# Optimization experiments

Measured on AMD Instinct MI355X. Metric: run time of the kernel, lower is better.

Reference implementation:

```python
import jax, jax.numpy as jnp
import numpy as np

B, CIN, COUT, WDIM, RES, K = 16, 512, 512, 512, 64, 3
LRELU_SLOPE = 0.2
ACT_GAIN = np.sqrt(2.0).astype(np.float32)  # def_gain for 'lrelu'


def setup_inputs() -> dict:
    key = jax.random.key(0)
    ks = jax.random.split(key, 7)
    return {
        "x": jax.random.normal(ks[0], (B, CIN, RES, RES), dtype=jnp.float32),
        "w": jax.random.normal(ks[1], (B, WDIM), dtype=jnp.float32),
        "weight": jax.random.normal(ks[2], (COUT, CIN, K, K), dtype=jnp.float32),
        "affine_w": jax.random.normal(ks[3], (CIN, WDIM), dtype=jnp.float32),
        "affine_b": jnp.ones((CIN,), dtype=jnp.float32),  # bias_init=1
        "bias": jnp.zeros((COUT,), dtype=jnp.float32),
        "noise_const": jax.random.normal(ks[4], (RES, RES), dtype=jnp.float32),
        "noise_strength": jnp.float32(0.1),
    }


def reference(x, w, weight, affine_w, affine_b, bias, noise_const, noise_strength):
    # affine: FullyConnectedLayer with weight_gain = 1/sqrt(w_dim)
    wg = jnp.float32(1.0 / np.sqrt(WDIM))
    styles = w @ (affine_w * wg).T + affine_b  # [B, CIN]

    # fused modulated conv2d (demodulate=True, fused_modconv=True, up=down=1)
    wm = weight[None] * styles[:, None, :, None, None]  # [B, COUT, CIN, K, K]
    dcoefs = jax.lax.rsqrt(jnp.sum(wm * wm, axis=(2, 3, 4)) + 1e-8)  # [B, COUT]
    wm = wm * dcoefs[:, :, None, None, None]

    # grouped conv trick: groups = batch
    xg = x.reshape(1, B * CIN, RES, RES)
    wgk = wm.reshape(B * COUT, CIN, K, K)
    pad = K // 2
    y = jax.lax.conv_general_dilated(
        xg, wgk, window_strides=(1, 1), padding=[(pad, pad), (pad, pad)],
        dimension_numbers=("NCHW", "OIHW", "NCHW"), feature_group_count=B,
    ).reshape(B, COUT, RES, RES)

    # const noise injection
    y = y + noise_const * noise_strength

    # bias_act: bias + leaky_relu + gain (conv_clamp=None, gain=1.0)
    y = jax.nn.leaky_relu(y + bias[None, :, None, None], LRELU_SLOPE) * ACT_GAIN
    return y
```

## Files before the change

kernel.cpp:

```cpp
#include <hip/hip_runtime.h>

#define BATCH 16
#define CIN 512
#define COUT 512
#define RES 64

typedef __attribute__((ext_vector_type(8))) short bf16x8;
typedef __attribute__((ext_vector_type(4))) float f32x4;

__device__ __align__(16) unsigned short g_zero[64];

static __device__ __forceinline__ unsigned short f2bf(float f) {
    unsigned int u = __float_as_uint(f);
    u += 0x7fffu + ((u >> 16) & 1u);
    return (unsigned short)(u >> 16);
}

static __device__ __forceinline__ void gload16(const void* g, void* l) {
    __builtin_amdgcn_global_load_lds(
        (const __attribute__((address_space(1))) void*)g,
        (__attribute__((address_space(3))) void*)l, 16, 0, 0);
}

__global__ void k_prep1(const float* __restrict__ w, const float* __restrict__ aw,
                        const float* __restrict__ ab, const float* __restrict__ weight,
                        float* __restrict__ styles, unsigned short* __restrict__ wA,
                        float* __restrict__ wsq) {
    if (blockIdx.x < 2048) {
        int wid  = (blockIdx.x * blockDim.x + threadIdx.x) >> 6;
        int lane = threadIdx.x & 63;
        int b = wid >> 9, i = wid & 511;
        const float* wrow = w + b * 512;
        const float* arow = aw + (size_t)i * 512;
        float acc = 0.f;
        for (int k = lane; k < 512; k += 64) acc += wrow[k] * arow[k];
        for (int off = 32; off; off >>= 1) acc += __shfl_down(acc, off, 64);
        if (lane == 0) styles[wid] = acc * 0.04419417382415922f + ab[i];
    } else {
        int o = blockIdx.x - 2048;
        __shared__ float lw[4608];
        for (int idx = threadIdx.x; idx < 4608; idx += 256)
            lw[idx] = weight[(size_t)o * 4608 + idx];
        __syncthreads();
        int i = threadIdx.x * 2;
        float sq0 = 0.f, sq1 = 0.f;
#pragma unroll
        for (int t = 0; t < 9; ++t) {
            float v0 = lw[i * 9 + t], v1 = lw[(i + 1) * 9 + t];
            sq0 += v0 * v0; sq1 += v1 * v1;
            unsigned* dst = (unsigned*)(wA + (((size_t)t * COUT + o) << 9));
            dst[threadIdx.x] = (unsigned)f2bf(v0) | ((unsigned)f2bf(v1) << 16);
        }
        *(float2*)(wsq + ((size_t)o << 9) + i) = make_float2(sq0, sq1);
    }
}

__global__ void k_dcoefs(const float* __restrict__ wsq, const float* __restrict__ styles,
                         float* __restrict__ dcoefs) {
    int wid  = (blockIdx.x * blockDim.x + threadIdx.x) >> 6;
    int lane = threadIdx.x & 63;
    int b = wid >> 9, o = wid & 511;
    const float* srow = styles + b * 512;
    const float* qrow = wsq + ((size_t)o << 9);
    float acc = 0.f;
    for (int i = lane; i < 512; i += 64) {
        float s = srow[i];
        acc += s * s * qrow[i];
    }
    for (int off = 32; off; off >>= 1) acc += __shfl_down(acc, off, 64);
    if (lane == 0) dcoefs[wid] = rsqrtf(acc + 1e-8f);
}

__global__ void k_xpose(const float* __restrict__ x, const float* __restrict__ styles,
                        unsigned short* __restrict__ xt) {
    int bh = blockIdx.x;
    int ic = blockIdx.y;
    int b = bh >> 6, h = bh & 63;
    __shared__ float tile[32][65];
    __shared__ float st[32];
    const float* src = x + ((size_t)b * 512 + ic * 32) * 4096 + h * 64;
    if (threadIdx.x < 32) st[threadIdx.x] = styles[b * 512 + ic * 32 + threadIdx.x];
    for (int idx = threadIdx.x; idx < 512; idx += 256) {
        int c = idx >> 4, w4 = (idx & 15) * 4;
        float4 v = *(const float4*)(src + (size_t)c * 4096 + w4);
        tile[c][w4] = v.x; tile[c][w4 + 1] = v.y; tile[c][w4 + 2] = v.z; tile[c][w4 + 3] = v.w;
    }
    __syncthreads();
    int w = threadIdx.x >> 2, cg = (threadIdx.x & 3) * 8;
    bf16x8 v;
#pragma unroll
    for (int j = 0; j < 8; ++j) v[j] = (short)f2bf(tile[cg + j][w] * st[cg + j]);
    *(bf16x8*)(xt + (((size_t)bh * 64 + w) << 9) + ic * 32 + cg) = v;
}

__global__ __launch_bounds__(256, 2)
void k_conv(const unsigned short* __restrict__ wA, const unsigned short* __restrict__ xt,
            const float* __restrict__ dcoefs,
            const float* __restrict__ noise, const float* __restrict__ nstr,
            const float* __restrict__ bias, float* __restrict__ out) {
    __shared__ __align__(16) unsigned short lA[128 * 32];
    __shared__ __align__(16) unsigned short lB[128 * 32];
    const int tid = threadIdx.x;
    const int lane = tid & 63;
    const int wave = tid >> 6;

    const int lid = blockIdx.x;
    const int xcd = lid & 7, grp = lid >> 3;
    const int o_blk = grp & 3;
    const int pair = ((grp >> 2) << 3) | xcd;
    const int b = pair >> 5;
    const int o0 = o_blk * 128;
    const int p0 = (pair & 31) * 128;
    const int h0 = p0 >> 6;

    const int kqs = (lane & 3) ^ ((lane >> 3) & 3);

    const unsigned short* gA0 = wA + ((size_t)(o0 + wave * 32 + (lane >> 2))) * 512 + kqs * 8;
    const unsigned short* gA1 = gA0 + 16 * 512;
    void* ldsA0 = (void*)(lA + wave * 1024);
    void* ldsA1 = (void*)(lA + wave * 1024 + 512);
    void* ldsB0 = (void*)(lB + wave * 1024);
    void* ldsB1 = (void*)(lB + wave * 1024 + 512);

    const int fm_row = (wave >> 1) * 64 + (lane & 15);
    const int fn_row = (wave & 1) * 64 + (lane & 15);
    const int kof = (((lane >> 4) ^ ((lane >> 1) & 3)) & 3) * 8;

    f32x4 acc[4][4];
#pragma unroll
    for (int i = 0; i < 4; ++i)
#pragma unroll
        for (int j = 0; j < 4; ++j) acc[i][j] = (f32x4){0.f, 0.f, 0.f, 0.f};

    for (int t = 0; t < 9; ++t) {
        const int dy = t / 3 - 1, dx = t % 3 - 1;
        const unsigned short* gB[2];
        int adv[2];
#pragma unroll
        for (int s = 0; s < 2; ++s) {
            int pp = wave * 32 + s * 16 + (lane >> 2);
            int r = pp >> 6, w = pp & 63;
            int h = h0 + r + dy, ww = w + dx;
            bool valid = ((unsigned)h < 64u) && ((unsigned)ww < 64u);
            gB[s] = valid ? xt + (((size_t)b * 64 + h) * 64 + ww) * 512 + kqs * 8
                          : g_zero + kqs * 8;
            adv[s] = valid ? 32 : 0;
        }
        for (int i0 = 0; i0 < 16; ++i0) {
            __syncthreads();
            gload16(gA0, ldsA0);
            gload16(gA1, ldsA1);
            gload16(gB[0], ldsB0);
            gload16(gB[1], ldsB1);
            gA0 += 32; gA1 += 32; gB[0] += adv[0]; gB[1] += adv[1];
            asm volatile("s_waitcnt vmcnt(0)" ::: "memory");
            __syncthreads();

            bf16x8 af[4], bfr[4];
#pragma unroll
            for (int f = 0; f < 4; ++f)
                af[f] = *(const bf16x8*)&lA[(fm_row + f * 16) * 32 + kof];
#pragma unroll
            for (int f = 0; f < 4; ++f)
                bfr[f] = *(const bf16x8*)&lB[(fn_row + f * 16) * 32 + kof];
#pragma unroll
            for (int fm = 0; fm < 4; ++fm)
#pragma unroll
                for (int fn = 0; fn < 4; ++fn)
                    acc[fm][fn] = __builtin_amdgcn_mfma_f32_16x16x32_bf16(
                        af[fm], bfr[fn], acc[fm][fn], 0, 0, 0);
        }
        gA0 += 261632; gA1 += 261632;
    }

    const float ns = nstr[0];
    const float* dcb = dcoefs + b * 512;
#pragma unroll
    for (int fm = 0; fm < 4; ++fm) {
        int ob = o0 + (wave >> 1) * 64 + fm * 16 + (lane >> 4) * 4;
#pragma unroll
        for (int fn = 0; fn < 4; ++fn) {
            int p = p0 + (wave & 1) * 64 + fn * 16 + (lane & 15);
            float nval = noise[p] * ns;
#pragma unroll
            for (int rg = 0; rg < 4; ++rg) {
                int o = ob + rg;
                float v = acc[fm][fn][rg] * dcb[o] + nval + bias[o];
                v = (v > 0.f ? v : 0.2f * v) * 1.41421356f;
                out[((size_t)(b * COUT + o) << 12) + p] = v;
            }
        }
    }
}

__global__ void k_conv_naive(const float* __restrict__ x, const float* __restrict__ w,
                             const float* __restrict__ weight,
                             const float* __restrict__ aw, const float* __restrict__ ab,
                             const float* __restrict__ noise, const float* __restrict__ nstr,
                             const float* __restrict__ bias, float* __restrict__ out) {
    const int o = blockIdx.x, b = blockIdx.y;
    __shared__ float ss[512];
    __shared__ float red[256];
    const float* wv = w + b * 512;
    for (int i = threadIdx.x; i < 512; i += 256) {
        const float* arow = aw + (size_t)i * 512;
        float acc = 0.f;
        for (int k = 0; k < 512; ++k) acc += wv[k] * arow[k];
        ss[i] = acc * 0.04419417382415922f + ab[i];
    }
    __syncthreads();
    float part = 0.f;
    for (int i = threadIdx.x; i < 512; i += 256) {
        float s = ss[i], sq = 0.f;
#pragma unroll
        for (int k = 0; k < 9; ++k) { float v = weight[((size_t)o * 512 + i) * 9 + k]; sq += v * v; }
        part += s * s * sq;
    }
    red[threadIdx.x] = part;
    __syncthreads();
    for (int st = 128; st; st >>= 1) {
        if (threadIdx.x < st) red[threadIdx.x] += red[threadIdx.x + st];
        __syncthreads();
    }
    const float dcoef = rsqrtf(red[0] + 1e-8f);

    float acc[16];
#pragma unroll
    for (int j = 0; j < 16; ++j) acc[j] = 0.f;
    for (int i = 0; i < 512; ++i) {
        const float s = ss[i];
        float wk[9];
#pragma unroll
        for (int k = 0; k < 9; ++k) wk[k] = weight[((size_t)o * 512 + i) * 9 + k] * s;
        const float* xp = x + ((size_t)b * 512 + i) * 4096;
#pragma unroll
        for (int j = 0; j < 16; ++j) {
            const int p = (j << 8) + threadIdx.x;
            const int h = p >> 6, ww = p & 63;
            float a = acc[j];
#pragma unroll
            for (int ky = 0; ky < 3; ++ky) {
                int hh = h + ky - 1;
                if ((unsigned)hh < 64u) {
#pragma unroll
                    for (int kx = 0; kx < 3; ++kx) {
                        int wv2 = ww + kx - 1;
                        if ((unsigned)wv2 < 64u) a += wk[ky * 3 + kx] * xp[hh * 64 + wv2];
                    }
                }
            }
            acc[j] = a;
        }
    }
    const float ns = nstr[0], bs = bias[o];
#pragma unroll
    for (int j = 0; j < 16; ++j) {
        int p = (j << 8) + threadIdx.x;
        float v = acc[j] * dcoef + noise[p] * ns + bs;
        v = (v > 0.f ? v : 0.2f * v) * 1.41421356f;
        out[((size_t)(b * COUT + o) << 12) + p] = v;
    }
}

extern "C" void kernel_launch(void* const* d_in, const int* in_sizes, int n_in,
                              void* d_out, int out_size, void* d_ws, size_t ws_size,
                              hipStream_t stream) {
    const float* x   = (const float*)d_in[0];
    const float* w   = (const float*)d_in[1];
    const float* wt  = (const float*)d_in[2];
    const float* aw  = (const float*)d_in[3];
    const float* ab  = (const float*)d_in[4];
    const float* bs  = (const float*)d_in[5];
    const float* nc  = (const float*)d_in[6];
    const float* nst = (const float*)d_in[7];
    float* out = (float*)d_out;

    char* ws = (char*)d_ws;
    float* styles = (float*)ws;
    float* dcoefs = (float*)(ws + 32 * 1024);
    float* wsq    = (float*)(ws + 64 * 1024);
    unsigned short* wA = (unsigned short*)(ws + (2 << 20));
    unsigned short* xt = (unsigned short*)(ws + (2 << 20) + 4718592ull);
    const size_t need = (size_t)(2 << 20) + 4718592ull + 67108864ull;

    if (d_ws != nullptr && ws_size >= need) {
        k_prep1<<<2560, 256, 0, stream>>>(w, aw, ab, wt, styles, wA, wsq);
        k_dcoefs<<<2048, 256, 0, stream>>>(wsq, styles, dcoefs);
        k_xpose<<<dim3(1024, 16), 256, 0, stream>>>(x, styles, xt);
        k_conv<<<2048, 256, 0, stream>>>(wA, xt, dcoefs, nc, nst, bs, out);
    } else {
        k_conv_naive<<<dim3(512, 16), 256, 0, stream>>>(x, w, wt, aw, ab, nc, nst, bs, out);
    }
}
```

Measured before the change: 605.0 us.

## Rewrite conv GEMM as 256x256 tile with double-buffered LDS pipeline

The implicit-GEMM conv kernel now uses 512-thread blocks, each computing a 256x256 output tile with a K step of 64. LDS is double-buffered and the global-to-LDS loads for upcoming K tiles are interleaved with four MFMA quadrant phases, using s_setprio and explicit vmcnt waits. The aim is to hide load latency and raise arithmetic intensity per LDS byte, in place of the old single-buffered 128x128 tile that waited on every load. In exchange the kernel needs 128 KB of LDS per block, more accumulator registers, and only 512 blocks, which may reduce occupancy.

```diff
diff --git a/kernel.cpp b/kernel.cpp
--- a/kernel.cpp
+++ b/kernel.cpp
@@ -4,6 +4,7 @@
 #define CIN 512
 #define COUT 512
 #define RES 64
+#define K_TILES 72
 
 typedef __attribute__((ext_vector_type(8))) short bf16x8;
 typedef __attribute__((ext_vector_type(4))) float f32x4;
@@ -93,98 +94,184 @@
     *(bf16x8*)(xt + (((size_t)bh * 64 + w) << 9) + ic * 32 + cg) = v;
 }
 
-__global__ __launch_bounds__(256, 2)
+__global__ __launch_bounds__(512, 2)
 void k_conv(const unsigned short* __restrict__ wA, const unsigned short* __restrict__ xt,
             const float* __restrict__ dcoefs,
             const float* __restrict__ noise, const float* __restrict__ nstr,
             const float* __restrict__ bias, float* __restrict__ out) {
-    __shared__ __align__(16) unsigned short lA[128 * 32];
-    __shared__ __align__(16) unsigned short lB[128 * 32];
-    const int tid = threadIdx.x;
+    __shared__ __align__(16) unsigned short lA[2][2][8192];
+    __shared__ __align__(16) unsigned short lB[2][2][8192];
+
+    const int tid  = threadIdx.x;
     const int lane = tid & 63;
     const int wave = tid >> 6;
-
-    const int lid = blockIdx.x;
-    const int xcd = lid & 7, grp = lid >> 3;
-    const int o_blk = grp & 3;
-    const int pair = ((grp >> 2) << 3) | xcd;
-    const int b = pair >> 5;
-    const int o0 = o_blk * 128;
-    const int p0 = (pair & 31) * 128;
-    const int h0 = p0 >> 6;
-
-    const int kqs = (lane & 3) ^ ((lane >> 3) & 3);
-
-    const unsigned short* gA0 = wA + ((size_t)(o0 + wave * 32 + (lane >> 2))) * 512 + kqs * 8;
-    const unsigned short* gA1 = gA0 + 16 * 512;
-    void* ldsA0 = (void*)(lA + wave * 1024);
-    void* ldsA1 = (void*)(lA + wave * 1024 + 512);
-    void* ldsB0 = (void*)(lB + wave * 1024);
-    void* ldsB1 = (void*)(lB + wave * 1024 + 512);
-
-    const int fm_row = (wave >> 1) * 64 + (lane & 15);
-    const int fn_row = (wave & 1) * 64 + (lane & 15);
-    const int kof = (((lane >> 4) ^ ((lane >> 1) & 3)) & 3) * 8;
-
-    f32x4 acc[4][4];
-#pragma unroll
-    for (int i = 0; i < 4; ++i)
+    const int wm = wave >> 2;
+    const int wn = wave & 3;
+
+    const int orig  = blockIdx.x;
+    const int wgid  = (orig & 7) * 64 + (orig >> 3);
+    const int o_blk = wgid & 1;
+    const int ptile = wgid >> 1;
+    const int b     = ptile >> 4;
+    const int h0    = (ptile & 15) << 2;
+    const int o0    = o_blk * 256;
+
+    const int jrow  = tid >> 3;
+    const int qsrc8 = (((tid & 7) ^ (jrow & 7)) & 7) * 8;
+
+    const int a_row_byte = (wm * 64 + (lane & 15)) * 128;
+    const int b_row_byte = (wn * 32 + (lane & 15)) * 128;
+    const int q0_byte = ((((lane >> 4)) ^ (lane & 7)) & 7) * 16;
+    const int q1_byte = ((((lane >> 4) | 4) ^ (lane & 7)) & 7) * 16;
+
+    auto stage_a = [&](int d, int q, int ktt) {
+        const int t = ktt >> 3, i0 = (ktt & 7) << 6;
+        const unsigned short* g0 =
+            wA + (((size_t)(t * COUT + o0 + q * 64 + jrow)) << 9) + i0 + qsrc8;
+        char* lb = (char*)&lA[d][q][0] + wave * 1024;
+        gload16(g0, lb);
+        gload16(g0 + (128 << 9), lb + 8192);
+    };
+    auto stage_b = [&](int d, int q, int ktt) {
+        const int t = ktt >> 3, i0 = (ktt & 7) << 6;
+        const int dy = t / 3 - 1, dx = t - (t / 3) * 3 - 1;
+        const int ww = q * 32 + (jrow & 31) + dx;
+        const int hh = h0 + (jrow >> 5) + dy;
+        const bool wok = (unsigned)ww < 64u;
+        const unsigned short* gz = g_zero + qsrc8;
+        const unsigned short* p0 = (wok && (unsigned)hh < 64u)
+            ? xt + (((size_t)(b * 4096 + hh * 64 + ww)) << 9) + i0 + qsrc8 : gz;
+        const unsigned short* p1 = (wok && (unsigned)(hh + 2) < 64u)
+            ? xt + (((size_t)(b * 4096 + (hh + 2) * 64 + ww)) << 9) + i0 + qsrc8 : gz;
+        char* lb = (char*)&lB[d][q][0] + wave * 1024;
+        gload16(p0, lb);
+        gload16(p1, lb + 8192);
+    };
+
+    f32x4 acc[8][4];
+#pragma unroll
+    for (int i = 0; i < 8; ++i)
 #pragma unroll
         for (int j = 0; j < 4; ++j) acc[i][j] = (f32x4){0.f, 0.f, 0.f, 0.f};
 
-    for (int t = 0; t < 9; ++t) {
-        const int dy = t / 3 - 1, dx = t % 3 - 1;
-        const unsigned short* gB[2];
-        int adv[2];
-#pragma unroll
-        for (int s = 0; s < 2; ++s) {
-            int pp = wave * 32 + s * 16 + (lane >> 2);
-            int r = pp >> 6, w = pp & 63;
-            int h = h0 + r + dy, ww = w + dx;
-            bool valid = ((unsigned)h < 64u) && ((unsigned)ww < 64u);
-            gB[s] = valid ? xt + (((size_t)b * 64 + h) * 64 + ww) * 512 + kqs * 8
-                          : g_zero + kqs * 8;
-            adv[s] = valid ? 32 : 0;
-        }
-        for (int i0 = 0; i0 < 16; ++i0) {
-            __syncthreads();
-            gload16(gA0, ldsA0);
-            gload16(gA1, ldsA1);
-            gload16(gB[0], ldsB0);
-            gload16(gB[1], ldsB1);
-            gA0 += 32; gA1 += 32; gB[0] += adv[0]; gB[1] += adv[1];
+    stage_a(0, 0, 0); stage_b(0, 0, 0); stage_a(0, 1, 0); stage_b(0, 1, 0);
+    asm volatile("s_waitcnt vmcnt(4)" ::: "memory");
+    stage_a(1, 0, 1); stage_b(1, 0, 1); stage_a(1, 1, 1);
+    asm volatile("s_waitcnt vmcnt(6)" ::: "memory");
+    __builtin_amdgcn_s_barrier();
+
+    bf16x8 a_lo[4][2], a_hi[4][2], b_lo[2][2], b_hi[2][2];
+
+    for (int kt = 0; kt < K_TILES; ++kt) {
+        const int cur = kt & 1;
+        const char* baseA = (const char*)&lA[cur][0][0];
+        const char* baseB = (const char*)&lB[cur][0][0];
+
+#pragma unroll
+        for (int f = 0; f < 4; ++f) {
+            a_lo[f][0] = *(const bf16x8*)(baseA + a_row_byte + f * 2048 + q0_byte);
+            a_lo[f][1] = *(const bf16x8*)(baseA + a_row_byte + f * 2048 + q1_byte);
+        }
+#pragma unroll
+        for (int g = 0; g < 2; ++g) {
+            b_lo[g][0] = *(const bf16x8*)(baseB + b_row_byte + g * 2048 + q0_byte);
+            b_lo[g][1] = *(const bf16x8*)(baseB + b_row_byte + g * 2048 + q1_byte);
+        }
+        if (kt + 1 < K_TILES) stage_b(cur ^ 1, 1, kt + 1);
+        __builtin_amdgcn_s_barrier();
+        asm volatile("s_waitcnt lgkmcnt(0)" ::: "memory");
+        __builtin_amdgcn_sched_barrier(0);
+        __builtin_amdgcn_s_setprio(1);
+#pragma unroll
+        for (int f = 0; f < 4; ++f)
+#pragma unroll
+            for (int g = 0; g < 2; ++g) {
+                f32x4 c = acc[f][g];
+                c = __builtin_amdgcn_mfma_f32_16x16x32_bf16(a_lo[f][0], b_lo[g][0], c, 0, 0, 0);
+                c = __builtin_amdgcn_mfma_f32_16x16x32_bf16(a_lo[f][1], b_lo[g][1], c, 0, 0, 0);
+                acc[f][g] = c;
+            }
+        __builtin_amdgcn_s_setprio(0);
+        __builtin_amdgcn_s_barrier();
+
+#pragma unroll
+        for (int g = 0; g < 2; ++g) {
+            b_hi[g][0] = *(const bf16x8*)(baseB + 16384 + b_row_byte + g * 2048 + q0_byte);
+            b_hi[g][1] = *(const bf16x8*)(baseB + 16384 + b_row_byte + g * 2048 + q1_byte);
+        }
+        if (kt + 2 < K_TILES) stage_a(cur, 0, kt + 2);
+        __builtin_amdgcn_s_barrier();
+        asm volatile("s_waitcnt lgkmcnt(0)" ::: "memory");
+        __builtin_amdgcn_sched_barrier(0);
+        __builtin_amdgcn_s_setprio(1);
+#pragma unroll
+        for (int f = 0; f < 4; ++f)
+#pragma unroll
+            for (int g = 0; g < 2; ++g) {
+                f32x4 c = acc[f][2 + g];
+                c = __builtin_amdgcn_mfma_f32_16x16x32_bf16(a_lo[f][0], b_hi[g][0], c, 0, 0, 0);
+                c = __builtin_amdgcn_mfma_f32_16x16x32_bf16(a_lo[f][1], b_hi[g][1], c, 0, 0, 0);
+                acc[f][2 + g] = c;
+            }
+        __builtin_amdgcn_s_setprio(0);
+        __builtin_amdgcn_s_barrier();
+
+#pragma unroll
+        for (int f = 0; f < 4; ++f) {
+            a_hi[f][0] = *(const bf16x8*)(baseA + 16384 + a_row_byte + f * 2048 + q0_byte);
+            a_hi[f][1] = *(const bf16x8*)(baseA + 16384 + a_row_byte + f * 2048 + q1_byte);
+        }
+        if (kt + 2 < K_TILES) stage_b(cur, 0, kt + 2);
+        __builtin_amdgcn_s_barrier();
+        asm volatile("s_waitcnt lgkmcnt(0)" ::: "memory");
+        __builtin_amdgcn_sched_barrier(0);
+        __builtin_amdgcn_s_setprio(1);
+#pragma unroll
+        for (int f = 0; f < 4; ++f)
+#pragma unroll
+            for (int g = 0; g < 2; ++g) {
+                f32x4 c = acc[4 + f][2 + g];
+                c = __builtin_amdgcn_mfma_f32_16x16x32_bf16(a_hi[f][0], b_hi[g][0], c, 0, 0, 0);
+                c = __builtin_amdgcn_mfma_f32_16x16x32_bf16(a_hi[f][1], b_hi[g][1], c, 0, 0, 0);
+                acc[4 + f][2 + g] = c;
+            }
+        __builtin_amdgcn_s_setprio(0);
+        __builtin_amdgcn_s_barrier();
+
+        if (kt + 2 < K_TILES) {
+            stage_a(cur, 1, kt + 2);
+            asm volatile("s_waitcnt vmcnt(6)" ::: "memory");
+        } else if (kt + 1 < K_TILES) {
             asm volatile("s_waitcnt vmcnt(0)" ::: "memory");
-            __syncthreads();
-
-            bf16x8 af[4], bfr[4];
-#pragma unroll
-            for (int f = 0; f < 4; ++f)
-                af[f] = *(const bf16x8*)&lA[(fm_row + f * 16) * 32 + kof];
-#pragma unroll
-            for (int f = 0; f < 4; ++f)
-                bfr[f] = *(const bf16x8*)&lB[(fn_row + f * 16) * 32 + kof];
-#pragma unroll
-            for (int fm = 0; fm < 4; ++fm)
-#pragma unroll
-                for (int fn = 0; fn < 4; ++fn)
-                    acc[fm][fn] = __builtin_amdgcn_mfma_f32_16x16x32_bf16(
-                        af[fm], bfr[fn], acc[fm][fn], 0, 0, 0);
-        }
-        gA0 += 261632; gA1 += 261632;
+        }
+        __builtin_amdgcn_s_barrier();
+        __builtin_amdgcn_s_setprio(1);
+#pragma unroll
+        for (int f = 0; f < 4; ++f)
+#pragma unroll
+            for (int g = 0; g < 2; ++g) {
+                f32x4 c = acc[4 + f][g];
+                c = __builtin_amdgcn_mfma_f32_16x16x32_bf16(a_hi[f][0], b_lo[g][0], c, 0, 0, 0);
+                c = __builtin_amdgcn_mfma_f32_16x16x32_bf16(a_hi[f][1], b_lo[g][1], c, 0, 0, 0);
+                acc[4 + f][g] = c;
+            }
+        __builtin_amdgcn_s_setprio(0);
+        __builtin_amdgcn_s_barrier();
     }
 
     const float ns = nstr[0];
     const float* dcb = dcoefs + b * 512;
-#pragma unroll
-    for (int fm = 0; fm < 4; ++fm) {
-        int ob = o0 + (wave >> 1) * 64 + fm * 16 + (lane >> 4) * 4;
+    const int pbase = (ptile & 15) * 256 + wn * 64 + (lane & 15);
+#pragma unroll
+    for (int fm = 0; fm < 8; ++fm) {
+        const int ob = o0 + wm * 128 + fm * 16 + ((lane >> 4) << 2);
 #pragma unroll
         for (int fn = 0; fn < 4; ++fn) {
-            int p = p0 + (wave & 1) * 64 + fn * 16 + (lane & 15);
-            float nval = noise[p] * ns;
+            const int p = pbase + fn * 16;
+            const float nval = noise[p] * ns;
 #pragma unroll
             for (int rg = 0; rg < 4; ++rg) {
-                int o = ob + rg;
+                const int o = ob + rg;
                 float v = acc[fm][fn][rg] * dcb[o] + nval + bias[o];
                 v = (v > 0.f ? v : 0.2f * v) * 1.41421356f;
                 out[((size_t)(b * COUT + o) << 12) + p] = v;
@@ -287,7 +374,7 @@
         k_prep1<<<2560, 256, 0, stream>>>(w, aw, ab, wt, styles, wA, wsq);
         k_dcoefs<<<2048, 256, 0, stream>>>(wsq, styles, dcoefs);
         k_xpose<<<dim3(1024, 16), 256, 0, stream>>>(x, styles, xt);
-        k_conv<<<2048, 256, 0, stream>>>(wA, xt, dcoefs, nc, nst, bs, out);
+        k_conv<<<512, 512, 0, stream>>>(wA, xt, dcoefs, nc, nst, bs, out);
     } else {
         k_conv_naive<<<dim3(512, 16), 256, 0, stream>>>(x, w, wt, aw, ab, nc, nst, bs, out);
     }
```

Result: faster. 528.4 us (-12.7%).

## Enlarge conv tiles to 256x256 with double-buffered LDS pipeline and rework transpose

Applied to the files above, without the earlier changes.

The implicit-GEMM conv kernel moves from 128x128 tiles with 256 threads to 256x256 tiles with 512 threads and a 64-wide K step. Global-to-LDS loads are double buffered, so the next tile is fetched while MFMAs run on the current one. Fragment reads are interleaved with MFMA groups under sched_barrier and setprio. This aims to cut barrier stalls and raise arithmetic intensity per block. The epilogue stages dcoefs and bias in LDS. The transpose kernel now handles all 512 channels per block with a swizzled packed store. The tradeoff is about 128KB of LDS per conv block, which limits occupancy to one block per CU, and only 512 blocks in the grid.

```diff
diff --git a/kernel.cpp b/kernel.cpp
--- a/kernel.cpp
+++ b/kernel.cpp
@@ -4,6 +4,7 @@
 #define CIN 512
 #define COUT 512
 #define RES 64
+#define K_TILES 72
 
 typedef __attribute__((ext_vector_type(8))) short bf16x8;
 typedef __attribute__((ext_vector_type(4))) float f32x4;
@@ -71,126 +72,234 @@
     if (lane == 0) dcoefs[wid] = rsqrtf(acc + 1e-8f);
 }
 
-__global__ void k_xpose(const float* __restrict__ x, const float* __restrict__ styles,
-                        unsigned short* __restrict__ xt) {
+__global__ __launch_bounds__(512) void k_xpose(const float* __restrict__ x,
+                                               const float* __restrict__ styles,
+                                               unsigned short* __restrict__ xt) {
     int bh = blockIdx.x;
-    int ic = blockIdx.y;
     int b = bh >> 6, h = bh & 63;
-    __shared__ float tile[32][65];
-    __shared__ float st[32];
-    const float* src = x + ((size_t)b * 512 + ic * 32) * 4096 + h * 64;
-    if (threadIdx.x < 32) st[threadIdx.x] = styles[b * 512 + ic * 32 + threadIdx.x];
-    for (int idx = threadIdx.x; idx < 512; idx += 256) {
+    __shared__ float tile[512][65];
+    __shared__ float st[512];
+    const int tid = threadIdx.x;
+    st[tid] = styles[b * 512 + tid];
+    __syncthreads();
+    const float* src = x + ((size_t)b * 512) * 4096 + h * 64;
+#pragma unroll
+    for (int it = 0; it < 16; ++it) {
+        int idx = it * 512 + tid;
         int c = idx >> 4, w4 = (idx & 15) * 4;
         float4 v = *(const float4*)(src + (size_t)c * 4096 + w4);
-        tile[c][w4] = v.x; tile[c][w4 + 1] = v.y; tile[c][w4 + 2] = v.z; tile[c][w4 + 3] = v.w;
+        float s = st[c];
+        tile[c][w4] = v.x * s; tile[c][w4 + 1] = v.y * s;
+        tile[c][w4 + 2] = v.z * s; tile[c][w4 + 3] = v.w * s;
     }
     __syncthreads();
-    int w = threadIdx.x >> 2, cg = (threadIdx.x & 3) * 8;
-    bf16x8 v;
-#pragma unroll
-    for (int j = 0; j < 8; ++j) v[j] = (short)f2bf(tile[cg + j][w] * st[cg + j]);
-    *(bf16x8*)(xt + (((size_t)bh * 64 + w) << 9) + ic * 32 + cg) = v;
-}
-
-__global__ __launch_bounds__(256, 2)
+    const int w = tid >> 3, l3 = tid & 7;
+    unsigned short* outp = xt + (((size_t)bh * 64 + w) << 9) + l3 * 64;
+#pragma unroll
+    for (int g = 0; g < 8; ++g) {
+        int bb = (g ^ l3) * 8;
+        int c0 = l3 * 64 + bb;
+        unsigned pk0 = (unsigned)f2bf(tile[c0 + 0][w]) | ((unsigned)f2bf(tile[c0 + 1][w]) << 16);
+        unsigned pk1 = (unsigned)f2bf(tile[c0 + 2][w]) | ((unsigned)f2bf(tile[c0 + 3][w]) << 16);
+        unsigned pk2 = (unsigned)f2bf(tile[c0 + 4][w]) | ((unsigned)f2bf(tile[c0 + 5][w]) << 16);
+        unsigned pk3 = (unsigned)f2bf(tile[c0 + 6][w]) | ((unsigned)f2bf(tile[c0 + 7][w]) << 16);
+        *(uint4*)(outp + bb) = make_uint4(pk0, pk1, pk2, pk3);
+    }
+}
+
+__global__ __launch_bounds__(512, 2)
 void k_conv(const unsigned short* __restrict__ wA, const unsigned short* __restrict__ xt,
             const float* __restrict__ dcoefs,
             const float* __restrict__ noise, const float* __restrict__ nstr,
             const float* __restrict__ bias, float* __restrict__ out) {
-    __shared__ __align__(16) unsigned short lA[128 * 32];
-    __shared__ __align__(16) unsigned short lB[128 * 32];
-    const int tid = threadIdx.x;
+    __shared__ __align__(16) unsigned short lA[2][16384];
+    __shared__ __align__(16) unsigned short lB[2][16384];
+    __shared__ float sdc[256];
+    __shared__ float sbias[256];
+
+    const int tid  = threadIdx.x;
     const int lane = tid & 63;
     const int wave = tid >> 6;
-
-    const int lid = blockIdx.x;
-    const int xcd = lid & 7, grp = lid >> 3;
-    const int o_blk = grp & 3;
-    const int pair = ((grp >> 2) << 3) | xcd;
-    const int b = pair >> 5;
-    const int o0 = o_blk * 128;
-    const int p0 = (pair & 31) * 128;
-    const int h0 = p0 >> 6;
-
-    const int kqs = (lane & 3) ^ ((lane >> 3) & 3);
-
-    const unsigned short* gA0 = wA + ((size_t)(o0 + wave * 32 + (lane >> 2))) * 512 + kqs * 8;
-    const unsigned short* gA1 = gA0 + 16 * 512;
-    void* ldsA0 = (void*)(lA + wave * 1024);
-    void* ldsA1 = (void*)(lA + wave * 1024 + 512);
-    void* ldsB0 = (void*)(lB + wave * 1024);
-    void* ldsB1 = (void*)(lB + wave * 1024 + 512);
-
-    const int fm_row = (wave >> 1) * 64 + (lane & 15);
-    const int fn_row = (wave & 1) * 64 + (lane & 15);
-    const int kof = (((lane >> 4) ^ ((lane >> 1) & 3)) & 3) * 8;
-
-    f32x4 acc[4][4];
-#pragma unroll
-    for (int i = 0; i < 4; ++i)
+    const int wm = wave >> 2;
+    const int wn = wave & 3;
+
+    const int orig  = blockIdx.x;
+    const int wgid  = (orig & 7) * 64 + (orig >> 3);
+    const int o_blk = wgid & 1;
+    const int ptile = wgid >> 1;
+    const int b     = ptile >> 4;
+    const int h0    = (ptile & 15) << 2;
+    const int o0    = o_blk * 256;
+    const int p0    = (ptile & 15) << 8;
+
+    const int srow  = tid >> 3;
+    const int qsrc8 = ((tid & 7) ^ (srow & 7)) * 8;
+
+    const int l7 = lane & 7;
+    const int a_off = (wm * 128 + (lane & 15)) * 128;
+    const int b_off = (wn * 64  + (lane & 15)) * 128;
+    const int qk0 = (((lane >> 4)    ) ^ l7) * 16;
+    const int qk1 = (((lane >> 4) | 4) ^ l7) * 16;
+
+    const unsigned short* pA;
+    const unsigned short* pB[4];
+    int aB[4];
+
+    auto recompA = [&](int ktt) {
+        pA = wA + (((size_t)((ktt >> 3) * COUT + o0 + srow)) << 9)
+                + ((ktt & 7) << 6) + qsrc8;
+    };
+    auto recompB = [&](int ktt) {
+        int tap = ktt >> 3;
+        int ty = tap / 3;
+        int dy = ty - 1, dx = tap - ty * 3 - 1;
+        int wv = srow + dx;
+        bool wok = (unsigned)wv < 64u;
+        int i0 = (ktt & 7) << 6;
+#pragma unroll
+        for (int s = 0; s < 4; ++s) {
+            int hh = h0 + s + dy;
+            bool ok = wok && ((unsigned)hh < 64u);
+            pB[s] = ok ? xt + (((size_t)(b * 4096 + hh * 64 + wv)) << 9) + i0 + qsrc8
+                       : g_zero + qsrc8;
+            aB[s] = ok ? 64 : 0;
+        }
+    };
+    auto stageA = [&](int d) {
+        char* lb = (char*)&lA[d][0] + wave * 1024;
+        gload16(pA,               lb);
+        gload16(pA + (64  << 9),  lb + 8192);
+        gload16(pA + (128 << 9),  lb + 16384);
+        gload16(pA + (192 << 9),  lb + 24576);
+    };
+    auto stageB = [&](int d) {
+        char* lb = (char*)&lB[d][0] + wave * 1024;
+        gload16(pB[0], lb);
+        gload16(pB[1], lb + 8192);
+        gload16(pB[2], lb + 16384);
+        gload16(pB[3], lb + 24576);
+    };
+
+    bf16x8 afr[2][4], bfr[2][4];
+    f32x4 acc[8][4];
+#pragma unroll
+    for (int i = 0; i < 8; ++i)
 #pragma unroll
         for (int j = 0; j < 4; ++j) acc[i][j] = (f32x4){0.f, 0.f, 0.f, 0.f};
 
-    for (int t = 0; t < 9; ++t) {
-        const int dy = t / 3 - 1, dx = t % 3 - 1;
-        const unsigned short* gB[2];
-        int adv[2];
-#pragma unroll
-        for (int s = 0; s < 2; ++s) {
-            int pp = wave * 32 + s * 16 + (lane >> 2);
-            int r = pp >> 6, w = pp & 63;
-            int h = h0 + r + dy, ww = w + dx;
-            bool valid = ((unsigned)h < 64u) && ((unsigned)ww < 64u);
-            gB[s] = valid ? xt + (((size_t)b * 64 + h) * 64 + ww) * 512 + kqs * 8
-                          : g_zero + kqs * 8;
-            adv[s] = valid ? 32 : 0;
-        }
-        for (int i0 = 0; i0 < 16; ++i0) {
-            __syncthreads();
-            gload16(gA0, ldsA0);
-            gload16(gA1, ldsA1);
-            gload16(gB[0], ldsB0);
-            gload16(gB[1], ldsB1);
-            gA0 += 32; gA1 += 32; gB[0] += adv[0]; gB[1] += adv[1];
+#define RD_A(S, H, QK, BASE) do {                                            \
+    afr[S][0] = *(const bf16x8*)((BASE) + a_off + ((H)*4 + 0)*2048 + (QK));  \
+    afr[S][1] = *(const bf16x8*)((BASE) + a_off + ((H)*4 + 1)*2048 + (QK));  \
+    afr[S][2] = *(const bf16x8*)((BASE) + a_off + ((H)*4 + 2)*2048 + (QK));  \
+    afr[S][3] = *(const bf16x8*)((BASE) + a_off + ((H)*4 + 3)*2048 + (QK));  \
+} while (0)
+#define RD_B(S, QK, BASE) do {                                               \
+    bfr[S][0] = *(const bf16x8*)((BASE) + b_off + 0*2048 + (QK));            \
+    bfr[S][1] = *(const bf16x8*)((BASE) + b_off + 1*2048 + (QK));            \
+    bfr[S][2] = *(const bf16x8*)((BASE) + b_off + 2*2048 + (QK));            \
+    bfr[S][3] = *(const bf16x8*)((BASE) + b_off + 3*2048 + (QK));            \
+} while (0)
+#define MM(AS, BS, H) do {                                                   \
+    _Pragma("unroll")                                                        \
+    for (int _j = 0; _j < 4; ++_j) {                                         \
+        _Pragma("unroll")                                                    \
+        for (int _fn = 0; _fn < 4; ++_fn)                                    \
+            acc[(H)*4 + _j][_fn] = __builtin_amdgcn_mfma_f32_16x16x32_bf16(  \
+                afr[AS][_j], bfr[BS][_fn], acc[(H)*4 + _j][_fn], 0, 0, 0);   \
+    }                                                                        \
+} while (0)
+
+    recompA(0); recompB(0); stageA(0); stageB(0);
+    recompA(1); recompB(1); stageA(1); stageB(1);
+    recompA(2); recompB(2);
+    asm volatile("s_waitcnt vmcnt(8)" ::: "memory");
+    __builtin_amdgcn_s_barrier();
+    {
+        const char* bA0 = (const char*)&lA[0][0];
+        const char* bB0 = (const char*)&lB[0][0];
+        RD_A(0, 0, qk0, bA0);
+        RD_B(0, qk0, bB0);
+    }
+
+    for (int kt = 0; kt < K_TILES; ++kt) {
+        const int cur = kt & 1;
+        const char* bA = (const char*)&lA[cur][0];
+        const char* bB = (const char*)&lB[cur][0];
+        const char* nA = (const char*)&lA[cur ^ 1][0];
+        const char* nB = (const char*)&lB[cur ^ 1][0];
+
+        RD_A(1, 1, qk0, bA);
+        __builtin_amdgcn_sched_barrier(0);
+        __builtin_amdgcn_s_setprio(1);
+        MM(0, 0, 0);
+        __builtin_amdgcn_s_setprio(0);
+
+        RD_A(0, 0, qk1, bA);
+        RD_B(1, qk1, bB);
+        __builtin_amdgcn_sched_barrier(0);
+        __builtin_amdgcn_s_setprio(1);
+        MM(1, 0, 1);
+        __builtin_amdgcn_s_setprio(0);
+
+        RD_A(1, 1, qk1, bA);
+        __builtin_amdgcn_sched_barrier(0);
+        __builtin_amdgcn_s_setprio(1);
+        MM(0, 1, 0);
+        __builtin_amdgcn_s_setprio(0);
+        asm volatile("s_waitcnt lgkmcnt(0)" ::: "memory");
+        __builtin_amdgcn_s_barrier();
+
+        if (kt + 2 < K_TILES) {
+            stageA(cur); stageB(cur);
+            int nk = kt + 3;
+            if (nk < K_TILES) {
+                if ((nk & 7) == 0) { recompA(nk); recompB(nk); }
+                else {
+                    pA += 64;
+                    pB[0] += aB[0]; pB[1] += aB[1]; pB[2] += aB[2]; pB[3] += aB[3];
+                }
+            }
+            asm volatile("s_waitcnt vmcnt(8)" ::: "memory");
+        } else {
             asm volatile("s_waitcnt vmcnt(0)" ::: "memory");
-            __syncthreads();
-
-            bf16x8 af[4], bfr[4];
-#pragma unroll
-            for (int f = 0; f < 4; ++f)
-                af[f] = *(const bf16x8*)&lA[(fm_row + f * 16) * 32 + kof];
-#pragma unroll
-            for (int f = 0; f < 4; ++f)
-                bfr[f] = *(const bf16x8*)&lB[(fn_row + f * 16) * 32 + kof];
-#pragma unroll
-            for (int fm = 0; fm < 4; ++fm)
-#pragma unroll
-                for (int fn = 0; fn < 4; ++fn)
-                    acc[fm][fn] = __builtin_amdgcn_mfma_f32_16x16x32_bf16(
-                        af[fm], bfr[fn], acc[fm][fn], 0, 0, 0);
-        }
-        gA0 += 261632; gA1 += 261632;
-    }
-
+        }
+        __builtin_amdgcn_s_barrier();
+        if (kt + 1 < K_TILES) {
+            RD_A(0, 0, qk0, nA);
+            RD_B(0, qk0, nB);
+        }
+        __builtin_amdgcn_sched_barrier(0);
+        __builtin_amdgcn_s_setprio(1);
+        MM(1, 1, 1);
+        __builtin_amdgcn_s_setprio(0);
+    }
+
+    if (tid < 256) {
+        sdc[tid]   = dcoefs[b * 512 + o0 + tid];
+        sbias[tid] = bias[o0 + tid];
+    }
+    __syncthreads();
     const float ns = nstr[0];
-    const float* dcb = dcoefs + b * 512;
-#pragma unroll
-    for (int fm = 0; fm < 4; ++fm) {
-        int ob = o0 + (wave >> 1) * 64 + fm * 16 + (lane >> 4) * 4;
+    const int prow = (lane >> 4) * 4;
+#pragma unroll
+    for (int fm = 0; fm < 8; ++fm) {
+        const int ob = wm * 128 + fm * 16 + prow;
 #pragma unroll
         for (int fn = 0; fn < 4; ++fn) {
-            int p = p0 + (wave & 1) * 64 + fn * 16 + (lane & 15);
-            float nval = noise[p] * ns;
+            const int p = p0 + wn * 64 + fn * 16 + (lane & 15);
+            const float nv = noise[p] * ns;
 #pragma unroll
             for (int rg = 0; rg < 4; ++rg) {
-                int o = ob + rg;
-                float v = acc[fm][fn][rg] * dcb[o] + nval + bias[o];
+                const int oo = ob + rg;
+                float v = acc[fm][fn][rg] * sdc[oo] + nv + sbias[oo];
                 v = (v > 0.f ? v : 0.2f * v) * 1.41421356f;
-                out[((size_t)(b * COUT + o) << 12) + p] = v;
+                out[((size_t)(b * COUT + o0 + oo) << 12) + p] = v;
             }
         }
     }
+#undef RD_A
+#undef RD_B
+#undef MM
 }
 
 __global__ void k_conv_naive(const float* __restrict__ x, const float* __restrict__ w,
@@ -286,8 +395,8 @@
     if (d_ws != nullptr && ws_size >= need) {
         k_prep1<<<2560, 256, 0, stream>>>(w, aw, ab, wt, styles, wA, wsq);
         k_dcoefs<<<2048, 256, 0, stream>>>(wsq, styles, dcoefs);
-        k_xpose<<<dim3(1024, 16), 256, 0, stream>>>(x, styles, xt);
-        k_conv<<<2048, 256, 0, stream>>>(wA, xt, dcoefs, nc, nst, bs, out);
+        k_xpose<<<1024, 512, 0, stream>>>(x, styles, xt);
+        k_conv<<<512, 512, 0, stream>>>(wA, xt, dcoefs, nc, nst, bs, out);
     } else {
         k_conv_naive<<<dim3(512, 16), 256, 0, stream>>>(x, w, wt, aw, ab, nc, nst, bs, out);
     }
```

After: 538.8 us. 10.9% less time.
